# Performance work log

Measured on AMD Instinct MI355X. Metric: run time of the kernel, lower is better.

The kernel has to match this reference:

```python
import jax, jax.numpy as jnp
import numpy as np

B, LS, VS = 4, 1024, 1024
VH, LH, H = 1024, 1024, 16
HD = LH // H  # head_dim = 64


def setup_inputs() -> dict:
    key = jax.random.key(0)
    ks = jax.random.split(key, 10)
    s = 0.02
    return {
        "v_hidden_states": jax.random.normal(ks[0], (B, VS, VH), jnp.float32),
        "l_hidden_states": jax.random.normal(ks[1], (B, LS, LH), jnp.float32),
        "q_w": jax.random.normal(ks[2], (LH, LH), jnp.float32) * s,
        "q_b": jnp.zeros((LH,), jnp.float32),
        "k_w": jax.random.normal(ks[3], (VH, LH), jnp.float32) * s,
        "k_b": jnp.zeros((LH,), jnp.float32),
        "v_w": jax.random.normal(ks[4], (VH, LH), jnp.float32) * s,
        "v_b": jnp.zeros((LH,), jnp.float32),
        "o_w": jax.random.normal(ks[5], (LH, LH), jnp.float32) * s,
        "o_b": jnp.zeros((LH,), jnp.float32),
    }


def reference(v_hidden_states, l_hidden_states, q_w, q_b, k_w, k_b, v_w, v_b, o_w, o_b):
    b, ls, _ = l_hidden_states.shape
    vs = v_hidden_states.shape[1]
    q = (l_hidden_states @ q_w + q_b).reshape(b, ls, H, HD)
    k = (v_hidden_states @ k_w + k_b).reshape(b, vs, H, HD)
    v = (v_hidden_states @ v_w + v_b).reshape(b, vs, H, HD)
    # NOTE: original scales by sqrt(hidden_size), not sqrt(head_dim)
    scale = jnp.sqrt(jnp.asarray(LH, q.dtype))
    scores = jnp.einsum("blhd,bvhd->bhlv", q, k) / scale
    attn = jax.nn.softmax(scores, axis=-1)
    out = jnp.einsum("bhlv,bvhd->blhd", attn, v).reshape(b, ls, LH)
    return out @ o_w + o_b
```

## Files before the change

### kernel.cpp

```cpp
#include <hip/hip_runtime.h>

typedef __bf16 bf16;
typedef __attribute__((ext_vector_type(4))) __bf16 bf16x4;
typedef __attribute__((ext_vector_type(8))) __bf16 bf16x8;
typedef __attribute__((ext_vector_type(4))) float f32x4;

static __device__ __forceinline__ f32x4 mfma_16x16x32(bf16x8 a, bf16x8 b, f32x4 c) {
    return __builtin_amdgcn_mfma_f32_16x16x32_bf16(a, b, c, 0, 0, 0);
}

static __device__ __forceinline__ bf16x8 load8(const float* p) {
    f32x4 a = *(const f32x4*)p;
    f32x4 b = *(const f32x4*)(p + 4);
    bf16x8 r;
    r[0] = (bf16)a[0]; r[1] = (bf16)a[1]; r[2] = (bf16)a[2]; r[3] = (bf16)a[3];
    r[4] = (bf16)b[0]; r[5] = (bf16)b[1]; r[6] = (bf16)b[2]; r[7] = (bf16)b[3];
    return r;
}

static __device__ __forceinline__ void gload_lds16(const void* g, void* l) {
    __builtin_amdgcn_global_load_lds(
        (const __attribute__((address_space(1))) void*)g,
        (__attribute__((address_space(3))) void*)l, 16, 0, 0);
}

__global__ __launch_bounds__(256) void prep_kernel(
    const float* __restrict__ l_h, const float* __restrict__ v_h,
    const float* __restrict__ w0, const float* __restrict__ w1,
    const float* __restrict__ w2, const float* __restrict__ w3,
    bf16* __restrict__ l_bf, bf16* __restrict__ v_bf,
    bf16* __restrict__ dq, bf16* __restrict__ dkv, bf16* __restrict__ dov)
{
    const int id = blockIdx.x;
    if (id < 4096) {
        const float* s = (id < 2048) ? l_h : v_h;
        bf16*       d = (id < 2048) ? l_bf : v_bf;
        const int   bb = (id < 2048) ? id : id - 2048;
        const size_t i = ((size_t)bb * 256 + threadIdx.x) * 8;
        *(bf16x8*)(d + i) = load8(s + i);
        return;
    }
    const int widx = id - 4096;
    const int z    = widx >> 8;
    const int rem  = widx & 255;
    const int j0   = (rem & 15) * 64;
    const int i0   = (rem >> 4) * 64;
    const float* src; bf16* dst;
    switch (z) {
        case 0:  src = w0; dst = dq; break;
        case 1:  src = w1; dst = dkv; break;
        case 2:  src = w2; dst = dkv + (size_t)1024 * 1024; break;
        default: src = w3; dst = dov; break;
    }
    const float wscale = (z == 0) ? 0.03125f : 1.0f;
    __shared__ float T[64][65];
    const int tx = threadIdx.x & 15;
    const int ty = threadIdx.x >> 4;
    #pragma unroll
    for (int it = 0; it < 4; ++it) {
        f32x4 v = *(const f32x4*)(src + (size_t)(i0 + ty + it * 16) * 1024 + j0 + tx * 4);
        T[ty + it * 16][tx * 4 + 0] = v[0];
        T[ty + it * 16][tx * 4 + 1] = v[1];
        T[ty + it * 16][tx * 4 + 2] = v[2];
        T[ty + it * 16][tx * 4 + 3] = v[3];
    }
    __syncthreads();
    #pragma unroll
    for (int it = 0; it < 4; ++it) {
        const int jj = ty + it * 16;
        bf16x4 o;
        o[0] = (bf16)(T[tx * 4 + 0][jj] * wscale);
        o[1] = (bf16)(T[tx * 4 + 1][jj] * wscale);
        o[2] = (bf16)(T[tx * 4 + 2][jj] * wscale);
        o[3] = (bf16)(T[tx * 4 + 3][jj] * wscale);
        *(bf16x4*)(dst + (size_t)(j0 + jj) * 1024 + i0 + tx * 4) = o;
    }
}

__global__ __launch_bounds__(256, 2) void proj128_kernel(
    const bf16* __restrict__ l_bf, const bf16* __restrict__ v_bf,
    const bf16* __restrict__ QWt,  const bf16* __restrict__ KVWt,
    const float* __restrict__ q_b, const float* __restrict__ k_b,
    const float* __restrict__ v_b,
    bf16* __restrict__ Qh, bf16* __restrict__ Kh, bf16* __restrict__ Vt)
{
    __shared__ __align__(16) bf16 As[128][32];
    __shared__ __align__(16) bf16 Bs[128][32];

    const int t    = threadIdx.x;
    const int lane = t & 63;
    const int wave = t >> 6;
    const int wm   = wave & 1;
    const int wn   = wave >> 1;
    const int l15  = lane & 15;
    const int quad = lane >> 4;

    const bool isQ = blockIdx.x < 8;
    const bf16* A  = isQ ? l_bf : v_bf;
    const bf16* Bt = isQ ? QWt  : KVWt;
    const int  gn0 = (isQ ? blockIdx.x : blockIdx.x - 8) * 128;
    const int  gm0 = blockIdx.y * 128;
    const int  K   = 1024;

    const int srow    = lane >> 2;
    const int chunk_g = (lane & 3) ^ ((srow >> 1) & 3);
    const size_t aoff = (size_t)(gm0 + wave * 32 + srow) * K + chunk_g * 8;
    const size_t boff = (size_t)(gn0 + wave * 32 + srow) * K + chunk_g * 8;

    f32x4 acc[4][4];
    #pragma unroll
    for (int i = 0; i < 4; ++i)
        #pragma unroll
        for (int j = 0; j < 4; ++j)
            acc[i][j] = (f32x4){0.f, 0.f, 0.f, 0.f};

    for (int k0 = 0; k0 < K; k0 += 32) {
        #pragma unroll
        for (int q = 0; q < 2; ++q) {
            gload_lds16(A  + aoff + (size_t)q * 16 * K + k0, &As[wave * 32 + q * 16][0]);
            gload_lds16(Bt + boff + (size_t)q * 16 * K + k0, &Bs[wave * 32 + q * 16][0]);
        }
        __syncthreads();

        bf16x8 af[4], bfr[4];
        #pragma unroll
        for (int mt = 0; mt < 4; ++mt) {
            const int row = wm * 64 + mt * 16 + l15;
            af[mt] = *(const bf16x8*)(&As[row][(quad ^ ((row >> 1) & 3)) * 8]);
        }
        #pragma unroll
        for (int nt = 0; nt < 4; ++nt) {
            const int row = wn * 64 + nt * 16 + l15;
            bfr[nt] = *(const bf16x8*)(&Bs[row][(quad ^ ((row >> 1) & 3)) * 8]);
        }
        #pragma unroll
        for (int mt = 0; mt < 4; ++mt)
            #pragma unroll
            for (int nt = 0; nt < 4; ++nt)
                acc[mt][nt] = mfma_16x16x32(af[mt], bfr[nt], acc[mt][nt]);

        __syncthreads();
    }

    #pragma unroll
    for (int nt = 0; nt < 4; ++nt) {
        const int col = gn0 + wn * 64 + nt * 16 + l15;
        float bb; bf16* dst; bool hm;
        if (isQ)             { bb = q_b[col] * 0.03125f; dst = Qh; hm = true;  }
        else if (col < 1024) { bb = k_b[col];            dst = Kh; hm = true;  }
        else                 { bb = v_b[col - 1024];     dst = Vt; hm = false; }
        #pragma unroll
        for (int mt = 0; mt < 4; ++mt) {
            #pragma unroll
            for (int r = 0; r < 4; ++r) {
                const int row = gm0 + wm * 64 + mt * 16 + quad * 4 + r;
                const float v = acc[mt][nt][r] + bb;
                if (hm) {
                    const size_t idx =
                        ((size_t)((row >> 10) * 16 + (col >> 6)) * 1024 +
                         (row & 1023)) * 64 + (col & 63);
                    dst[idx] = (bf16)v;
                } else {
                    const int vc = col - 1024;
                    const size_t idx =
                        ((size_t)((row >> 10) * 16 + (vc >> 6)) * 64 +
                         (vc & 63)) * 1024 + (row & 1023);
                    dst[idx] = (bf16)v;
                }
            }
        }
    }
}

static __device__ __forceinline__ void gemm_core_128x64(
    const bf16* __restrict__ A, const bf16* __restrict__ Bt, int K,
    int gm0, int gn0, bf16 (*As)[32], bf16 (*Bs)[32], f32x4 acc[4][2])
{
    const int t    = threadIdx.x;
    const int lane = t & 63;
    const int wave = t >> 6;
    const int wm   = wave & 1;
    const int wn   = wave >> 1;
    const int l15  = lane & 15;
    const int quad = lane >> 4;

    const int srow    = lane >> 2;
    const int chunk_g = (lane & 3) ^ ((srow >> 1) & 3);
    const size_t aoff = (size_t)(gm0 + wave * 32 + srow) * K + chunk_g * 8;
    const size_t boff = (size_t)(gn0 + wave * 16 + srow) * K + chunk_g * 8;

    #pragma unroll
    for (int i = 0; i < 4; ++i)
        #pragma unroll
        for (int j = 0; j < 2; ++j)
            acc[i][j] = (f32x4){0.f, 0.f, 0.f, 0.f};

    for (int k0 = 0; k0 < K; k0 += 32) {
        gload_lds16(A + aoff + k0,                  &As[wave * 32][0]);
        gload_lds16(A + aoff + (size_t)16 * K + k0, &As[wave * 32 + 16][0]);
        gload_lds16(Bt + boff + k0,                 &Bs[wave * 16][0]);
        __syncthreads();

        bf16x8 af[4], bfr[2];
        #pragma unroll
        for (int mt = 0; mt < 4; ++mt) {
            const int row = wm * 64 + mt * 16 + l15;
            af[mt] = *(const bf16x8*)(&As[row][(quad ^ ((row >> 1) & 3)) * 8]);
        }
        #pragma unroll
        for (int nt = 0; nt < 2; ++nt) {
            const int row = wn * 32 + nt * 16 + l15;
            bfr[nt] = *(const bf16x8*)(&Bs[row][(quad ^ ((row >> 1) & 3)) * 8]);
        }
        #pragma unroll
        for (int mt = 0; mt < 4; ++mt)
            #pragma unroll
            for (int nt = 0; nt < 2; ++nt)
                acc[mt][nt] = mfma_16x16x32(af[mt], bfr[nt], acc[mt][nt]);

        __syncthreads();
    }
}

__global__ __launch_bounds__(256, 3) void ogemm_kernel(
    const bf16* __restrict__ Aw, const bf16* __restrict__ OWt,
    const float* __restrict__ o_b, float* __restrict__ C)
{
    __shared__ __align__(16) bf16 As[128][32];
    __shared__ __align__(16) bf16 Bs[64][32];

    const int gn0 = blockIdx.x * 64;
    const int gm0 = blockIdx.y * 128;

    f32x4 acc[4][2];
    gemm_core_128x64(Aw, OWt, 1024, gm0, gn0, As, Bs, acc);

    const int lane = threadIdx.x & 63;
    const int wave = threadIdx.x >> 6;
    const int wm   = wave & 1;
    const int wn   = wave >> 1;
    const int l15  = lane & 15;
    const int quad = lane >> 4;

    #pragma unroll
    for (int nt = 0; nt < 2; ++nt) {
        const int col = gn0 + wn * 32 + nt * 16 + l15;
        const float bb = o_b[col];
        #pragma unroll
        for (int mt = 0; mt < 4; ++mt) {
            #pragma unroll
            for (int r = 0; r < 4; ++r) {
                const int row = gm0 + wm * 64 + mt * 16 + quad * 4 + r;
                C[(size_t)row * 1024 + col] = acc[mt][nt][r] + bb;
            }
        }
    }
}

__global__ __launch_bounds__(256) void attn_kernel(
    const bf16* __restrict__ Q, const bf16* __restrict__ K,
    const bf16* __restrict__ V, bf16* __restrict__ O)
{
    const int t    = threadIdx.x;
    const int lane = t & 63;
    const int wave = t >> 6;
    const int l15  = lane & 15;
    const int quad = lane >> 4;

    const int head = blockIdx.x;
    const int q0   = blockIdx.y * 128;
    const int b    = head >> 4;
    const int h    = head & 15;

    __shared__ __align__(16) bf16 Kb[2][64][64];
    __shared__ __align__(16) bf16 Vb[2][64][64];
    __shared__ __align__(16) bf16 P[4][32][72];

    const bf16* Qp  = Q + ((size_t)head * 1024 + q0 + wave * 32) * 64;
    const bf16* Kp  = K + (size_t)head * 1024 * 64;
    const bf16* Vtp = V + (size_t)head * 64 * 1024;

    const int r8  = lane >> 3;
    const int c8  = lane & 7;
    const int swz = (c8 ^ r8) * 8;

    bf16x8 aq[2][2];
    #pragma unroll
    for (int mt = 0; mt < 2; ++mt)
        #pragma unroll
        for (int kc = 0; kc < 2; ++kc)
            aq[mt][kc] = *(const bf16x8*)(Qp + (mt * 16 + l15) * 64 + kc * 32 + quad * 8);

    f32x4 oacc[2][4];
    #pragma unroll
    for (int mt = 0; mt < 2; ++mt)
        #pragma unroll
        for (int nt = 0; nt < 4; ++nt)
            oacc[mt][nt] = (f32x4){0.f, 0.f, 0.f, 0.f};
    float lsum[2][4];
    #pragma unroll
    for (int mt = 0; mt < 2; ++mt)
        #pragma unroll
        for (int r = 0; r < 4; ++r) lsum[mt][r] = 0.f;

    #define STAGE(c, buf)                                                          \
        {                                                                          \
            const int kv0_ = (c) * 64;                                             \
            _Pragma("unroll")                                                      \
            for (int g = 0; g < 2; ++g) {                                          \
                const int R = wave * 16 + g * 8;                                   \
                gload_lds16(Kp + (size_t)(kv0_ + R + r8) * 64 + swz,               \
                            &Kb[buf][R][0]);                                       \
                gload_lds16(Vtp + (size_t)(R + r8) * 1024 + kv0_ + swz,            \
                            &Vb[buf][R][0]);                                       \
            }                                                                      \
        }

    STAGE(0, 0);

    const int sw = l15 & 7;

    for (int c = 0; c < 16; ++c) {
        const int buf = c & 1;
        __syncthreads();
        if (c + 1 < 16) STAGE(c + 1, buf ^ 1);

        #pragma unroll
        for (int nt = 0; nt < 4; ++nt) {
            const bf16* krow = &Kb[buf][nt * 16 + l15][0];
            bf16x8 bk0 = *(const bf16x8*)(krow + (quad ^ sw) * 8);
            bf16x8 bk1 = *(const bf16x8*)(krow + ((quad + 4) ^ sw) * 8);
            #pragma unroll
            for (int mt = 0; mt < 2; ++mt) {
                f32x4 s = (f32x4){0.f, 0.f, 0.f, 0.f};
                s = mfma_16x16x32(aq[mt][0], bk0, s);
                s = mfma_16x16x32(aq[mt][1], bk1, s);
                #pragma unroll
                for (int r = 0; r < 4; ++r) {
                    const float e = __expf(s[r]);
                    lsum[mt][r] += e;
                    P[wave][mt * 16 + quad * 4 + r][nt * 16 + l15] = (bf16)e;
                }
            }
        }

        #pragma unroll
        for (int mt = 0; mt < 2; ++mt) {
            bf16x8 pa0 = *(const bf16x8*)(&P[wave][mt * 16 + l15][quad * 8]);
            bf16x8 pa1 = *(const bf16x8*)(&P[wave][mt * 16 + l15][32 + quad * 8]);
            #pragma unroll
            for (int nt = 0; nt < 4; ++nt) {
                const bf16* vrow = &Vb[buf][nt * 16 + l15][0];
                bf16x8 bv0 = *(const bf16x8*)(vrow + (quad ^ sw) * 8);
                bf16x8 bv1 = *(const bf16x8*)(vrow + ((quad + 4) ^ sw) * 8);
                oacc[mt][nt] = mfma_16x16x32(pa0, bv0, oacc[mt][nt]);
                oacc[mt][nt] = mfma_16x16x32(pa1, bv1, oacc[mt][nt]);
            }
        }
    }
    #undef STAGE

    #pragma unroll
    for (int off = 1; off <= 8; off <<= 1)
        #pragma unroll
        for (int mt = 0; mt < 2; ++mt)
            #pragma unroll
            for (int r = 0; r < 4; ++r)
                lsum[mt][r] += __shfl_xor(lsum[mt][r], off, 64);

    #pragma unroll
    for (int mt = 0; mt < 2; ++mt) {
        const float invs[4] = {1.0f / lsum[mt][0], 1.0f / lsum[mt][1],
                               1.0f / lsum[mt][2], 1.0f / lsum[mt][3]};
        #pragma unroll
        for (int nt = 0; nt < 4; ++nt) {
            #pragma unroll
            for (int r = 0; r < 4; ++r) {
                const int row = q0 + wave * 32 + mt * 16 + quad * 4 + r;
                O[((size_t)b * 1024 + row) * 1024 + h * 64 + nt * 16 + l15] =
                    (bf16)(oacc[mt][nt][r] * invs[r]);
            }
        }
    }
}

extern "C" void kernel_launch(void* const* d_in, const int* in_sizes, int n_in,
                              void* d_out, int out_size, void* d_ws, size_t ws_size,
                              hipStream_t stream)
{
    const float* v_h = (const float*)d_in[0];
    const float* l_h = (const float*)d_in[1];
    const float* q_w = (const float*)d_in[2];
    const float* q_b = (const float*)d_in[3];
    const float* k_w = (const float*)d_in[4];
    const float* k_b = (const float*)d_in[5];
    const float* v_w = (const float*)d_in[6];
    const float* v_b = (const float*)d_in[7];
    const float* o_w = (const float*)d_in[8];
    const float* o_b = (const float*)d_in[9];
    float* out = (float*)d_out;

    const size_t SZ = (size_t)4096 * 1024;
    const size_t WZ = (size_t)1024 * 1024;

    bf16* l_bf = (bf16*)d_ws;
    bf16* v_bf = l_bf + SZ;
    bf16* QWt  = v_bf + SZ;
    bf16* KVWt = QWt + WZ;
    bf16* OWt  = KVWt + 2 * WZ;
    bf16* Qh   = OWt + WZ;
    bf16* Kh   = Qh + SZ;
    bf16* Vt   = Kh + SZ;
    bf16* Aw   = Vt + SZ;

    prep_kernel<<<dim3(5120), 256, 0, stream>>>(
        l_h, v_h, q_w, k_w, v_w, o_w, l_bf, v_bf, QWt, KVWt, OWt);

    proj128_kernel<<<dim3(24, 32), 256, 0, stream>>>(
        l_bf, v_bf, QWt, KVWt, q_b, k_b, v_b, Qh, Kh, Vt);

    attn_kernel<<<dim3(64, 8), 256, 0, stream>>>(Qh, Kh, Vt, Aw);

    ogemm_kernel<<<dim3(16, 32), 256, 0, stream>>>(Aw, OWt, o_b, out);

    (void)in_sizes; (void)n_in; (void)out_size; (void)ws_size;
}
```

Baseline: 195.5 us.

## Split-K output GEMM with 128x128 tiles and fold log2e into Q scale

The output projection moves from 128x64 tiles to 128x128 tiles with K split in two. Each half writes fp32 partials into dead workspace regions, and a separate reduce kernel sums them and adds the bias. The intent is more data reuse per tile while keeping the block count the same. The cost is an extra kernel launch and a full fp32 write and read of two partial buffers. Separately, log2(e) is folded into the Q weight and bias scale so the softmax can use exp2f instead of __expf, which saves a multiply per score.

```diff
diff --git a/kernel.cpp b/kernel.cpp
--- a/kernel.cpp
+++ b/kernel.cpp
@@ -23,6 +23,8 @@
         (const __attribute__((address_space(1))) void*)g,
         (__attribute__((address_space(3))) void*)l, 16, 0, 0);
 }
+
+#define QSCALE 0.0450842200277801f
 
 __global__ __launch_bounds__(256) void prep_kernel(
     const float* __restrict__ l_h, const float* __restrict__ v_h,
@@ -52,7 +54,7 @@
         case 2:  src = w2; dst = dkv + (size_t)1024 * 1024; break;
         default: src = w3; dst = dov; break;
     }
-    const float wscale = (z == 0) ? 0.03125f : 1.0f;
+    const float wscale = (z == 0) ? QSCALE : 1.0f;
     __shared__ float T[64][65];
     const int tx = threadIdx.x & 15;
     const int ty = threadIdx.x >> 4;
@@ -146,7 +148,7 @@
     for (int nt = 0; nt < 4; ++nt) {
         const int col = gn0 + wn * 64 + nt * 16 + l15;
         float bb; bf16* dst; bool hm;
-        if (isQ)             { bb = q_b[col] * 0.03125f; dst = Qh; hm = true;  }
+        if (isQ)             { bb = q_b[col] * QSCALE;   dst = Qh; hm = true;  }
         else if (col < 1024) { bb = k_b[col];            dst = Kh; hm = true;  }
         else                 { bb = v_b[col - 1024];     dst = Vt; hm = false; }
         #pragma unroll
@@ -172,10 +174,13 @@
     }
 }
 
-static __device__ __forceinline__ void gemm_core_128x64(
-    const bf16* __restrict__ A, const bf16* __restrict__ Bt, int K,
-    int gm0, int gn0, bf16 (*As)[32], bf16 (*Bs)[32], f32x4 acc[4][2])
-{
+__global__ __launch_bounds__(256, 2) void ogemm_split_kernel(
+    const bf16* __restrict__ Aw, const bf16* __restrict__ OWt,
+    float* __restrict__ P0, float* __restrict__ P1)
+{
+    __shared__ __align__(16) bf16 As[128][32];
+    __shared__ __align__(16) bf16 Bs[128][32];
+
     const int t    = threadIdx.x;
     const int lane = t & 63;
     const int wave = t >> 6;
@@ -184,77 +189,78 @@
     const int l15  = lane & 15;
     const int quad = lane >> 4;
 
+    const int gn0  = blockIdx.x * 128;
+    const int gm0  = blockIdx.y * 128;
+    const int K    = 1024;
+    const int koff = blockIdx.z * 512;
+    float* outp    = blockIdx.z ? P1 : P0;
+
     const int srow    = lane >> 2;
     const int chunk_g = (lane & 3) ^ ((srow >> 1) & 3);
-    const size_t aoff = (size_t)(gm0 + wave * 32 + srow) * K + chunk_g * 8;
-    const size_t boff = (size_t)(gn0 + wave * 16 + srow) * K + chunk_g * 8;
-
+    const size_t aoff = (size_t)(gm0 + wave * 32 + srow) * K + koff + chunk_g * 8;
+    const size_t boff = (size_t)(gn0 + wave * 32 + srow) * K + koff + chunk_g * 8;
+
+    f32x4 acc[4][4];
     #pragma unroll
     for (int i = 0; i < 4; ++i)
         #pragma unroll
-        for (int j = 0; j < 2; ++j)
+        for (int j = 0; j < 4; ++j)
             acc[i][j] = (f32x4){0.f, 0.f, 0.f, 0.f};
 
-    for (int k0 = 0; k0 < K; k0 += 32) {
-        gload_lds16(A + aoff + k0,                  &As[wave * 32][0]);
-        gload_lds16(A + aoff + (size_t)16 * K + k0, &As[wave * 32 + 16][0]);
-        gload_lds16(Bt + boff + k0,                 &Bs[wave * 16][0]);
+    for (int k0 = 0; k0 < 512; k0 += 32) {
+        #pragma unroll
+        for (int q = 0; q < 2; ++q) {
+            gload_lds16(Aw  + aoff + (size_t)q * 16 * K + k0, &As[wave * 32 + q * 16][0]);
+            gload_lds16(OWt + boff + (size_t)q * 16 * K + k0, &Bs[wave * 32 + q * 16][0]);
+        }
         __syncthreads();
 
-        bf16x8 af[4], bfr[2];
+        bf16x8 af[4], bfr[4];
         #pragma unroll
         for (int mt = 0; mt < 4; ++mt) {
             const int row = wm * 64 + mt * 16 + l15;
             af[mt] = *(const bf16x8*)(&As[row][(quad ^ ((row >> 1) & 3)) * 8]);
         }
         #pragma unroll
-        for (int nt = 0; nt < 2; ++nt) {
-            const int row = wn * 32 + nt * 16 + l15;
+        for (int nt = 0; nt < 4; ++nt) {
+            const int row = wn * 64 + nt * 16 + l15;
             bfr[nt] = *(const bf16x8*)(&Bs[row][(quad ^ ((row >> 1) & 3)) * 8]);
         }
         #pragma unroll
         for (int mt = 0; mt < 4; ++mt)
             #pragma unroll
-            for (int nt = 0; nt < 2; ++nt)
+            for (int nt = 0; nt < 4; ++nt)
                 acc[mt][nt] = mfma_16x16x32(af[mt], bfr[nt], acc[mt][nt]);
 
         __syncthreads();
     }
-}
-
-__global__ __launch_bounds__(256, 3) void ogemm_kernel(
-    const bf16* __restrict__ Aw, const bf16* __restrict__ OWt,
-    const float* __restrict__ o_b, float* __restrict__ C)
-{
-    __shared__ __align__(16) bf16 As[128][32];
-    __shared__ __align__(16) bf16 Bs[64][32];
-
-    const int gn0 = blockIdx.x * 64;
-    const int gm0 = blockIdx.y * 128;
-
-    f32x4 acc[4][2];
-    gemm_core_128x64(Aw, OWt, 1024, gm0, gn0, As, Bs, acc);
-
-    const int lane = threadIdx.x & 63;
-    const int wave = threadIdx.x >> 6;
-    const int wm   = wave & 1;
-    const int wn   = wave >> 1;
-    const int l15  = lane & 15;
-    const int quad = lane >> 4;
-
-    #pragma unroll
-    for (int nt = 0; nt < 2; ++nt) {
-        const int col = gn0 + wn * 32 + nt * 16 + l15;
-        const float bb = o_b[col];
+
+    #pragma unroll
+    for (int nt = 0; nt < 4; ++nt) {
+        const int col = gn0 + wn * 64 + nt * 16 + l15;
         #pragma unroll
         for (int mt = 0; mt < 4; ++mt) {
             #pragma unroll
             for (int r = 0; r < 4; ++r) {
                 const int row = gm0 + wm * 64 + mt * 16 + quad * 4 + r;
-                C[(size_t)row * 1024 + col] = acc[mt][nt][r] + bb;
+                outp[(size_t)row * 1024 + col] = acc[mt][nt][r];
             }
         }
     }
+}
+
+__global__ __launch_bounds__(256) void reduce_kernel(
+    const float* __restrict__ P0, const float* __restrict__ P1,
+    const float* __restrict__ o_b, float* __restrict__ C)
+{
+    const size_t i = ((size_t)blockIdx.x * 256 + threadIdx.x) * 4;
+    f32x4 a = *(const f32x4*)(P0 + i);
+    f32x4 b = *(const f32x4*)(P1 + i);
+    f32x4 bb = *(const f32x4*)(o_b + (i & 1023));
+    f32x4 o;
+    #pragma unroll
+    for (int j = 0; j < 4; ++j) o[j] = a[j] + b[j] + bb[j];
+    *(f32x4*)(C + i) = o;
 }
 
 __global__ __launch_bounds__(256) void attn_kernel(
@@ -337,7 +343,7 @@
                 s = mfma_16x16x32(aq[mt][1], bk1, s);
                 #pragma unroll
                 for (int r = 0; r < 4; ++r) {
-                    const float e = __expf(s[r]);
+                    const float e = exp2f(s[r]);
                     lsum[mt][r] += e;
                     P[wave][mt * 16 + quad * 4 + r][nt * 16 + l15] = (bf16)e;
                 }
@@ -413,6 +419,9 @@
     bf16* Vt   = Kh + SZ;
     bf16* Aw   = Vt + SZ;
 
+    float* KP0 = (float*)l_bf;
+    float* KP1 = (float*)Qh;
+
     prep_kernel<<<dim3(5120), 256, 0, stream>>>(
         l_h, v_h, q_w, k_w, v_w, o_w, l_bf, v_bf, QWt, KVWt, OWt);
 
@@ -421,7 +430,9 @@
 
     attn_kernel<<<dim3(64, 8), 256, 0, stream>>>(Qh, Kh, Vt, Aw);
 
-    ogemm_kernel<<<dim3(16, 32), 256, 0, stream>>>(Aw, OWt, o_b, out);
+    ogemm_split_kernel<<<dim3(8, 32, 2), 256, 0, stream>>>(Aw, OWt, KP0, KP1);
+
+    reduce_kernel<<<dim3(4096), 256, 0, stream>>>(KP0, KP1, o_b, out);
 
     (void)in_sizes; (void)n_in; (void)out_size; (void)ws_size;
 }
```

New measurement: 208.1 us. 1.06x slower.
